# Performance work log

Measured on AMD Instinct MI355X. Metric: run time of the kernel, lower is better.

## Reference

```python
import jax, jax.numpy as jnp
import numpy as np
from jax import lax

D = 64
ROWS, COLS = np.triu_indices(D)  # 2080 upper-triangular (row, col) pairs, row-major like the python loop
BN_S = 1.0 / np.sqrt(1.0 + 1e-5)  # inference BN with running_mean=0, running_var=1


def _bn_relu(x, g, b):
    # inference-mode BatchNorm2d (fresh running stats) followed by ReLU; x is NCHW
    return jax.nn.relu(x * (g * BN_S)[None, :, None, None] + b[None, :, None, None])


def _conv(x, w, stride, pad):
    return lax.conv_general_dilated(x, w, (stride, stride), [(pad, pad), (pad, pad)],
                                    dimension_numbers=('NCHW', 'OIHW', 'NCHW'))


def _block(x, g1, b1, w1, g2, b2, w2, stride, ws=None):
    xa = _bn_relu(x, g1, b1)
    y = _conv(xa, w1, stride, 1)
    y = _conv(_bn_relu(y, g2, b2), w2, 1, 1)
    sc = xa if ws is None else _conv(xa, ws, stride, 0)
    return y + sc


def _forward(x, y, conv_w, s1_g1, s1_b1, s1_w1, s1_g2, s1_b2, s1_w2,
             s2_g1, s2_b1, s2_w1, s2_g2, s2_b2, s2_w2, s2_ws,
             s3_g1, s3_b1, s3_w1, s3_g2, s3_b2, s3_w2, s3_ws,
             bn_g, bn_b, ct_w, ct_b):
    h = _conv(x, conv_w, 1, 1)                                   # (B,16,36,60)
    h = _block(h, s1_g1, s1_b1, s1_w1, s1_g2, s1_b2, s1_w2, 1)    # (B,16,36,60)
    h = _block(h, s2_g1, s2_b1, s2_w1, s2_g2, s2_b2, s2_w2, 2, s2_ws)  # (B,32,18,30)
    h = _block(h, s3_g1, s3_b1, s3_w1, s3_g2, s3_b2, s3_w2, 2, s3_ws)  # (B,64,9,15)
    h = _bn_relu(h, bn_g, bn_b)                                   # (B,64,9,15)
    xp = jnp.transpose(h, (0, 2, 3, 1))                           # (B,9,15,64) channels-last
    # triangular bilinear pooling: z[..., k] = x[..., row_k] * x[..., col_k]
    z = xp[..., ROWS] * xp[..., COLS]                             # (B,9,15,2080)
    # 1x1 conv d2 -> 64 ("condtoc") + channel gating
    A = jnp.einsum('bhwk,ok->bhwo', z, ct_w) + ct_b               # (B,9,15,64)
    G = jnp.mean(A, axis=(1, 2), keepdims=True)                   # (B,1,1,64) adaptive avg pool
    Dg = A * G + A
    out = xp * Dg + xp                                            # (B,9,15,64)
    return out


def setup_inputs() -> dict:
    key = jax.random.key(0)
    ks = iter(jax.random.split(key, 40))

    def rn(shape, scale=0.1):
        return jax.random.normal(next(ks), shape, dtype=jnp.float32) * scale

    def gm(shape):
        return jax.random.uniform(next(ks), shape, dtype=jnp.float32, minval=0.5, maxval=1.5)

    return {
        'x': rn((64, 3, 36, 60), 1.0), 'y': rn((64, 2), 1.0),
        'conv_w': rn((16, 3, 3, 3)),
        's1_g1': gm((16,)), 's1_b1': rn((16,)), 's1_w1': rn((16, 16, 3, 3)),
        's1_g2': gm((16,)), 's1_b2': rn((16,)), 's1_w2': rn((16, 16, 3, 3)),
        's2_g1': gm((16,)), 's2_b1': rn((16,)), 's2_w1': rn((32, 16, 3, 3)),
        's2_g2': gm((32,)), 's2_b2': rn((32,)), 's2_w2': rn((32, 32, 3, 3)),
        's2_ws': rn((32, 16, 1, 1)),
        's3_g1': gm((32,)), 's3_b1': rn((32,)), 's3_w1': rn((64, 32, 3, 3)),
        's3_g2': gm((64,)), 's3_b2': rn((64,)), 's3_w2': rn((64, 64, 3, 3)),
        's3_ws': rn((64, 32, 1, 1)),
        'bn_g': gm((64,)), 'bn_b': rn((64,)),
        'ct_w': rn((64, 2080), 0.02), 'ct_b': rn((64,), 0.02),
    }


def reference(x, y, conv_w, s1_g1, s1_b1, s1_w1, s1_g2, s1_b2, s1_w2,
              s2_g1, s2_b1, s2_w1, s2_g2, s2_b2, s2_w2, s2_ws,
              s3_g1, s3_b1, s3_w1, s3_g2, s3_b2, s3_w2, s3_ws,
              bn_g, bn_b, ct_w, ct_b):
    return _forward(x, y, conv_w, s1_g1, s1_b1, s1_w1, s1_g2, s1_b2, s1_w2,
                    s2_g1, s2_b1, s2_w1, s2_g2, s2_b2, s2_w2, s2_ws,
                    s3_g1, s3_b1, s3_w1, s3_g2, s3_b2, s3_w2, s3_ws,
                    bn_g, bn_b, ct_w, ct_b)
```

## Files before the change

### kernel.cpp

```cpp
#include <hip/hip_runtime.h>

#define BN_S 0.9999950000374997f

constexpr int BATCH = 64;

typedef __attribute__((ext_vector_type(8))) short bf16x8;
typedef __attribute__((ext_vector_type(4))) float f32x4;

__device__ __forceinline__ float bnrelu(float x, float gs, float bb) {
    return fmaxf(fmaf(x, gs, bb), 0.f);
}

__device__ __forceinline__ unsigned short f2bf(float f) {
    unsigned u = __builtin_bit_cast(unsigned, f);
    return (unsigned short)((u + 0x7FFFu + ((u >> 16) & 1u)) >> 16);
}
__device__ __forceinline__ float bf2f(unsigned short h) {
    unsigned u = ((unsigned)h) << 16;
    return __builtin_bit_cast(float, u);
}

template<int CIN, int CICH, int COUT, int CO_PER, int HIN, int WIN,
         int HOUT, int WOUT, int STRIDE, int ROWS, int P, int PARTS,
         bool PRE_BN, int SC, int CSC, int SSTR, int SCPARTS>
__global__ __launch_bounds__(256) void convT_k(
    const float* __restrict__ in, size_t in_pstride,
    const float* __restrict__ w,
    const float* __restrict__ g, const float* __restrict__ bb,
    const float* __restrict__ xin, size_t xin_pstride,
    const float* __restrict__ g1v, const float* __restrict__ b1v,
    const float* __restrict__ wsc,
    float* __restrict__ out, size_t out_pstride)
{
    constexpr int IR = (STRIDE == 1) ? ROWS + 2 : 2 * ROWS + 1;
    constexpr int TW = (STRIDE == 1) ? WIN + 2 : WIN + 1;
    constexpr int AW = (P - 1) * STRIDE + 3;
    constexpr int NCOG = COUT / CO_PER;
    constexpr int PGW = WOUT / P;
    constexpr int NG = ROWS * PGW;
    constexpr int NITEMS = NG * NCOG;

    __shared__ float xs[CICH * IR * TW];
    __shared__ float wlds[CICH * 9 * COUT];
    __shared__ float g1l[SC ? CSC : 1], b1l[SC ? CSC : 1];
    __shared__ float wscl[(SC == 2) ? CSC * COUT : 1];

    const int band = blockIdx.x, b = blockIdx.y, zci = blockIdx.z;
    const int ci0 = zci * CICH;
    const int r0 = band * ROWS;
    const int r0in = r0 * STRIDE - 1;
    const int tid = threadIdx.x;

    for (int i = tid; i < CICH * 9 * COUT; i += 256) {
        int co = i % COUT; int rem = i / COUT; int tap = rem % 9; int ci = rem / 9;
        wlds[i] = w[((size_t)co * CIN + ci0 + ci) * 9 + tap];
    }
    if constexpr (SC != 0) {
        if (tid < CSC) { g1l[tid] = g1v[tid] * BN_S; b1l[tid] = b1v[tid]; }
        if constexpr (SC == 2) {
            for (int i = tid; i < CSC * COUT; i += 256) {
                int co = i % COUT; int ci = i / COUT;
                wscl[i] = wsc[(size_t)co * CSC + ci];
            }
        }
    }
    for (int i = tid; i < CICH * IR * TW; i += 256) {
        int cc = i % TW; int rem = i / TW; int rr = rem % IR; int ci = rem / IR;
        int gr = r0in + rr; int gc = cc - 1;
        float v = 0.f;
        if (gr >= 0 && gr < HIN && gc >= 0 && gc < WIN) {
            size_t off = ((size_t)(b * CIN + ci0 + ci) * HIN + gr) * WIN + gc;
            v = in[off];
            if constexpr (PARTS >= 2) v += in[off + in_pstride];
            if constexpr (PARTS >= 3) v += in[off + 2 * in_pstride];
            if constexpr (PARTS >= 4) v += in[off + 3 * in_pstride];
            if constexpr (PRE_BN) v = bnrelu(v, g[ci0 + ci] * BN_S, bb[ci0 + ci]);
        }
        xs[i] = v;
    }
    __syncthreads();

    for (int it = tid; it < NITEMS; it += 256) {
        const int cog = it / NG; const int gi = it % NG;
        const int lr = gi / PGW; const int wc = (gi % PGW) * P;
        float acc[P][CO_PER];
#pragma unroll
        for (int j = 0; j < P; ++j)
#pragma unroll
            for (int co = 0; co < CO_PER; ++co) acc[j][co] = 0.f;

        for (int ci = 0; ci < CICH; ++ci) {
            const float* xb = xs + ((ci * IR) + lr * STRIDE) * TW + wc * STRIDE;
#pragma unroll
            for (int dh = 0; dh < 3; ++dh) {
                float aw[AW];
#pragma unroll
                for (int a = 0; a < AW; ++a) aw[a] = xb[dh * TW + a];
#pragma unroll
                for (int dw = 0; dw < 3; ++dw) {
                    const float* wp = wlds + (ci * 9 + dh * 3 + dw) * COUT + cog * CO_PER;
#pragma unroll
                    for (int c4 = 0; c4 < CO_PER; c4 += 4) {
                        float4 wv = *(const float4*)(wp + c4);
#pragma unroll
                        for (int j = 0; j < P; ++j) {
                            float a_ = aw[j * STRIDE + dw];
                            acc[j][c4 + 0] = fmaf(a_, wv.x, acc[j][c4 + 0]);
                            acc[j][c4 + 1] = fmaf(a_, wv.y, acc[j][c4 + 1]);
                            acc[j][c4 + 2] = fmaf(a_, wv.z, acc[j][c4 + 2]);
                            acc[j][c4 + 3] = fmaf(a_, wv.w, acc[j][c4 + 3]);
                        }
                    }
                }
            }
        }

        if constexpr (SC == 1) {
            if (zci == 0) {
#pragma unroll
                for (int co = 0; co < CO_PER; ++co) {
                    int c = cog * CO_PER + co;
#pragma unroll
                    for (int j = 0; j < P; ++j) {
                        size_t off = ((size_t)(b * CSC + c) * HOUT + (r0 + lr)) * WOUT + wc + j;
                        float v = xin[off];
#pragma unroll
                        for (int s = 1; s < SCPARTS; ++s) v += xin[off + s * xin_pstride];
                        acc[j][co] += bnrelu(v, g1l[c], b1l[c]);
                    }
                }
            }
        }
        if constexpr (SC == 2) {
            if (zci == 0) {
                const int hix = (r0 + lr) * SSTR;
                for (int ci = 0; ci < CSC; ++ci) {
                    float vv[P];
#pragma unroll
                    for (int j = 0; j < P; ++j) {
                        size_t off = ((size_t)(b * CSC + ci) * (HOUT * SSTR) + hix) * (WOUT * SSTR)
                                     + (wc + j) * SSTR;
                        float v = xin[off];
#pragma unroll
                        for (int s = 1; s < SCPARTS; ++s) v += xin[off + s * xin_pstride];
                        vv[j] = bnrelu(v, g1l[ci], b1l[ci]);
                    }
                    const float* wp = wscl + ci * COUT + cog * CO_PER;
#pragma unroll
                    for (int c4 = 0; c4 < CO_PER; c4 += 4) {
                        float4 wv = *(const float4*)(wp + c4);
#pragma unroll
                        for (int j = 0; j < P; ++j) {
                            acc[j][c4 + 0] = fmaf(vv[j], wv.x, acc[j][c4 + 0]);
                            acc[j][c4 + 1] = fmaf(vv[j], wv.y, acc[j][c4 + 1]);
                            acc[j][c4 + 2] = fmaf(vv[j], wv.z, acc[j][c4 + 2]);
                            acc[j][c4 + 3] = fmaf(vv[j], wv.w, acc[j][c4 + 3]);
                        }
                    }
                }
            }
        }

        float* op = out + (size_t)zci * out_pstride
                    + ((size_t)(b * COUT + cog * CO_PER) * HOUT + (r0 + lr)) * WOUT + wc;
#pragma unroll
        for (int co = 0; co < CO_PER; ++co)
#pragma unroll
            for (int j = 0; j < P; ++j)
                op[(size_t)co * HOUT * WOUT + j] = acc[j][co];
    }
}

__global__ void f0_k(const float* __restrict__ ctw, short* __restrict__ wf)
{
    int id = blockIdx.x * 256 + threadIdx.x;
    int j = id & 7; int lane = (id >> 3) & 63; int tile = (id >> 9) & 3; int s = id >> 11;
    int c, ch;
    if (s < 32) { c = s; ch = 0; }
    else { c = 32 + ((s - 32) >> 1); ch = (s - 32) & 1; }
    int k = ch * 32 + ((lane >> 4) << 3) + j;
    int o = tile * 16 + (lane & 15);
    float val = 0.f;
    if (k <= c) val = ctw[o * 2080 + (k * (129 - k)) / 2 + (c - k)];
    wf[id] = (short)f2bf(val);
}

__global__ __launch_bounds__(256) void red_k(
    const float* __restrict__ pb, const float* __restrict__ h2,
    const float* __restrict__ g1, const float* __restrict__ b1,
    const float* __restrict__ wsc, const float* __restrict__ bng,
    const float* __restrict__ bnb, float* __restrict__ xp)
{
    __shared__ float hsc[32][136];
    __shared__ float wscl[32][16];
    __shared__ float g1l[32], b1l[32];
    const int b = blockIdx.x, cq = blockIdx.y;
    const int c0 = cq * 16;
    const int t = threadIdx.x;

    if (t < 32) { g1l[t] = g1[t] * BN_S; b1l[t] = b1[t]; }
    for (int i = t; i < 512; i += 256) {
        int ci = i & 31, cc = i >> 5;
        wscl[ci][cc] = wsc[(size_t)(c0 + cc) * 32 + ci];
    }
    __syncthreads();
    for (int i = t; i < 32 * 135; i += 256) {
        int ci = i / 135, p = i % 135;
        int hp = p / 15, wp = p % 15;
        size_t off = ((size_t)(b * 32 + ci) * 18 + hp * 2) * 30 + wp * 2;
        float v = h2[off] + h2[off + 1105920] + h2[off + 2 * 1105920] + h2[off + 3 * 1105920];
        hsc[ci][p] = bnrelu(v, g1l[ci], b1l[ci]);
    }
    __syncthreads();

    for (int e = t; e < 16 * 135; e += 256) {
        int cc = e / 135, p = e % 135;
        int c = c0 + cc;
        size_t idx = ((size_t)(b * 64 + c)) * 135 + p;
        float y = 0.f;
#pragma unroll
        for (int q = 0; q < 8; ++q) y += pb[idx + (size_t)q * 552960];
#pragma unroll 8
        for (int ci = 0; ci < 32; ++ci) y = fmaf(hsc[ci][p], wscl[ci][cc], y);
        xp[((size_t)b * 135 + p) * 64 + c] = bnrelu(y, bng[c] * BN_S, bnb[c]);
    }
}

template<int NCH>
__device__ __forceinline__ void f2m_body(
    const unsigned short* xs, int q, const short* __restrict__ wf,
    const float* __restrict__ ctb, float* __restrict__ Abase, int p0, int t)
{
    float* A = Abase + (size_t)q * 552960;
    const int w = t >> 6, lane = t & 63;
    const int prow = w * 32;
    const int lrow = lane & 15, lk = lane >> 4;

    bf16x8 Af[2][NCH];
#pragma unroll
    for (int rt = 0; rt < 2; ++rt)
#pragma unroll
        for (int ch = 0; ch < NCH; ++ch) {
            int pix = prow + rt * 16 + lrow;
            int g = ch * 4 + lk;
            Af[rt][ch] = *(const bf16x8*)&xs[pix * 64 + ((g ^ (pix & 7)) * 8)];
        }

    f32x4 acc[2][4];
#pragma unroll
    for (int rt = 0; rt < 2; ++rt)
#pragma unroll
        for (int tt = 0; tt < 4; ++tt) acc[rt][tt] = f32x4{0.f, 0.f, 0.f, 0.f};

    const int c0 = q * 16;
    bf16x8 BA[NCH][4], BB[NCH][4];

    auto loadB = [&](int c, bf16x8 (&B)[NCH][4]) {
        int slotb = (NCH == 1) ? c : (2 * c - 32);
#pragma unroll
        for (int ch = 0; ch < NCH; ++ch) {
            const short* wb = wf + (size_t)(slotb + ch) * 2048 + lane * 8;
#pragma unroll
            for (int tt = 0; tt < 4; ++tt)
                B[ch][tt] = *(const bf16x8*)(wb + tt * 512);
        }
    };
    auto compute = [&](int c, bf16x8 (&B)[NCH][4]) {
        f32x4 S[2][4];
#pragma unroll
        for (int rt = 0; rt < 2; ++rt)
#pragma unroll
            for (int tt = 0; tt < 4; ++tt) S[rt][tt] = f32x4{0.f, 0.f, 0.f, 0.f};
#pragma unroll
        for (int ch = 0; ch < NCH; ++ch)
#pragma unroll
            for (int tt = 0; tt < 4; ++tt) {
                S[0][tt] = __builtin_amdgcn_mfma_f32_16x16x32_bf16(Af[0][ch], B[ch][tt], S[0][tt], 0, 0, 0);
                S[1][tt] = __builtin_amdgcn_mfma_f32_16x16x32_bf16(Af[1][ch], B[ch][tt], S[1][tt], 0, 0, 0);
            }
#pragma unroll
        for (int rt = 0; rt < 2; ++rt)
#pragma unroll
            for (int j = 0; j < 4; ++j) {
                int pix = prow + rt * 16 + lk * 4 + j;
                float sv = bf2f(xs[pix * 64 + (((c >> 3) ^ (pix & 7)) * 8) + (c & 7)]);
#pragma unroll
                for (int tt = 0; tt < 4; ++tt)
                    acc[rt][tt][j] += sv * S[rt][tt][j];
            }
    };

    loadB(c0, BA);
#pragma unroll 1
    for (int ci = 0; ci < 16; ci += 2) {
        loadB(c0 + ci + 1, BB);
        compute(c0 + ci, BA);
        if (ci < 14) loadB(c0 + ci + 2, BA);
        compute(c0 + ci + 1, BB);
    }

#pragma unroll
    for (int rt = 0; rt < 2; ++rt)
#pragma unroll
        for (int j = 0; j < 4; ++j) {
            int gpix = p0 + prow + rt * 16 + lk * 4 + j;
            if (gpix < 8640) {
#pragma unroll
                for (int tt = 0; tt < 4; ++tt) {
                    int o = tt * 16 + lrow;
                    float vv = acc[rt][tt][j];
                    if (q == 0) vv += ctb[o];
                    A[(size_t)gpix * 64 + o] = vv;
                }
            }
        }
}

__global__ __launch_bounds__(256) void f2m_k(
    const float* __restrict__ xp, const short* __restrict__ wf,
    const float* __restrict__ ctb, float* __restrict__ Abase)
{
    __shared__ unsigned short xs[128 * 64];
    const int t = threadIdx.x;
    const int p0 = blockIdx.x * 128;
    const int q = blockIdx.y;

    {
        int pr = t >> 1, h = t & 1;
        int gp = p0 + pr;
        float v[32];
        if (gp < 8640) {
            const float4* src = (const float4*)(xp + (size_t)gp * 64 + h * 32);
#pragma unroll
            for (int i = 0; i < 8; ++i) {
                float4 x4 = src[i];
                v[i*4+0] = x4.x; v[i*4+1] = x4.y; v[i*4+2] = x4.z; v[i*4+3] = x4.w;
            }
        } else {
#pragma unroll
            for (int i = 0; i < 32; ++i) v[i] = 0.f;
        }
#pragma unroll
        for (int g = 0; g < 4; ++g) {
            unsigned w0 = f2bf(v[g*8+0]) | ((unsigned)f2bf(v[g*8+1]) << 16);
            unsigned w1 = f2bf(v[g*8+2]) | ((unsigned)f2bf(v[g*8+3]) << 16);
            unsigned w2 = f2bf(v[g*8+4]) | ((unsigned)f2bf(v[g*8+5]) << 16);
            unsigned w3 = f2bf(v[g*8+6]) | ((unsigned)f2bf(v[g*8+7]) << 16);
            int grp = h * 4 + g;
            int sg = grp ^ (pr & 7);
            *(uint4*)&xs[pr * 64 + sg * 8] = make_uint4(w0, w1, w2, w3);
        }
    }
    __syncthreads();

    if (q < 2) f2m_body<1>(xs, q, wf, ctb, Abase, p0, t);
    else       f2m_body<2>(xs, q, wf, ctb, Abase, p0, t);
}

__global__ void f3a_k(const float* __restrict__ A, float* __restrict__ G)
{
    int b = blockIdx.x; int t = threadIdx.x;
    int o = t & 63; int grp = t >> 6;
    float s = 0.f;
    for (int p = grp; p < 135; p += 4) {
        size_t off = ((size_t)b * 135 + p) * 64 + o;
        s += A[off] + A[off + 552960] + A[off + 2 * 552960] + A[off + 3 * 552960];
    }
    __shared__ float red[4][64];
    red[grp][o] = s;
    __syncthreads();
    if (t < 64) G[b * 64 + t] = (red[0][t] + red[1][t] + red[2][t] + red[3][t]) * (1.0f / 135.0f);
}

__global__ void f3b_k(const float* __restrict__ xp, const float* __restrict__ A,
                      const float* __restrict__ G, float* __restrict__ out)
{
    int idx = blockIdx.x * 256 + threadIdx.x;
    if (idx >= BATCH * 135 * 64) return;
    int o = idx & 63; int b = idx / (135 * 64);
    float a = A[idx] + A[idx + 552960] + A[idx + 2 * 552960] + A[idx + 3 * 552960];
    float g = G[b * 64 + o];
    float x = xp[idx];
    out[idx] = fmaf(x, a * (g + 1.f), x);
}

extern "C" void kernel_launch(void* const* d_in, const int* in_sizes, int n_in,
                              void* d_out, int out_size, void* d_ws, size_t ws_size,
                              hipStream_t stream)
{
    const float* x      = (const float*)d_in[0];
    const float* conv_w = (const float*)d_in[2];
    const float* s1_g1  = (const float*)d_in[3];
    const float* s1_b1  = (const float*)d_in[4];
    const float* s1_w1  = (const float*)d_in[5];
    const float* s1_g2  = (const float*)d_in[6];
    const float* s1_b2  = (const float*)d_in[7];
    const float* s1_w2  = (const float*)d_in[8];
    const float* s2_g1  = (const float*)d_in[9];
    const float* s2_b1  = (const float*)d_in[10];
    const float* s2_w1  = (const float*)d_in[11];
    const float* s2_g2  = (const float*)d_in[12];
    const float* s2_b2  = (const float*)d_in[13];
    const float* s2_w2  = (const float*)d_in[14];
    const float* s2_ws  = (const float*)d_in[15];
    const float* s3_g1  = (const float*)d_in[16];
    const float* s3_b1  = (const float*)d_in[17];
    const float* s3_w1  = (const float*)d_in[18];
    const float* s3_g2  = (const float*)d_in[19];
    const float* s3_b2  = (const float*)d_in[20];
    const float* s3_w2  = (const float*)d_in[21];
    const float* s3_ws  = (const float*)d_in[22];
    const float* bn_g   = (const float*)d_in[23];
    const float* bn_b   = (const float*)d_in[24];
    const float* ct_w   = (const float*)d_in[25];
    const float* ct_b   = (const float*)d_in[26];
    float* out = (float*)d_out;

    float* ws = (float*)d_ws;
    float* h0      = ws + 0;
    float* p_b1c1  = ws + 2211840;
    float* h1      = ws + 11059200;
    float* p_b2c1  = ws + 0;
    float* p_b2c2  = ws + 4423680;
    float* p_b3c1  = ws + 0;
    float* p_b3c2  = ws + 8847360;
    float* xp      = ws + 0;
    float* A       = ws + 552960;
    float* G       = ws + 15482880;
    short* wfrag   = (short*)(ws + 15487232);

    dim3 blk(256);

    f0_k<<<768, blk, 0, stream>>>(ct_w, wfrag);

    convT_k<3, 3, 16, 8, 36, 60, 36, 60, 1, 6, 3, 1, false, 0, 1, 1, 1>
        <<<dim3(6, 64, 1), blk, 0, stream>>>(
        x, 0, conv_w, nullptr, nullptr, nullptr, 0, nullptr, nullptr, nullptr, h0, 0);
    convT_k<16, 4, 16, 8, 36, 60, 36, 60, 1, 9, 5, 1, true, 0, 1, 1, 1>
        <<<dim3(4, 64, 4), blk, 0, stream>>>(
        h0, 0, s1_w1, s1_g1, s1_b1, nullptr, 0, nullptr, nullptr, nullptr, p_b1c1, 2211840);
    convT_k<16, 8, 16, 8, 36, 60, 36, 60, 1, 9, 5, 4, true, 1, 16, 1, 1>
        <<<dim3(4, 64, 2), blk, 0, stream>>>(
        p_b1c1, 2211840, s1_w2, s1_g2, s1_b2, h0, 0, s1_g1, s1_b1, nullptr, h1, 2211840);
    convT_k<16, 4, 32, 8, 36, 60, 18, 30, 2, 6, 5, 2, true, 0, 1, 1, 1>
        <<<dim3(3, 64, 4), blk, 0, stream>>>(
        h1, 2211840, s2_w1, s2_g1, s2_b1, nullptr, 0, nullptr, nullptr, nullptr, p_b2c1, 1105920);
    convT_k<32, 8, 32, 8, 18, 30, 18, 30, 1, 6, 5, 4, true, 2, 16, 2, 2>
        <<<dim3(3, 64, 4), blk, 0, stream>>>(
        p_b2c1, 1105920, s2_w2, s2_g2, s2_b2, h1, 2211840, s2_g1, s2_b1, s2_ws, p_b2c2, 1105920);
    convT_k<32, 8, 64, 4, 18, 30, 9, 15, 2, 3, 3, 4, true, 0, 1, 1, 1>
        <<<dim3(3, 64, 4), blk, 0, stream>>>(
        p_b2c2, 1105920, s3_w1, s3_g1, s3_b1, nullptr, 0, nullptr, nullptr, nullptr, p_b3c1, 552960);
    convT_k<64, 8, 64, 4, 9, 15, 9, 15, 1, 3, 3, 4, true, 0, 1, 1, 1>
        <<<dim3(3, 64, 8), blk, 0, stream>>>(
        p_b3c1, 552960, s3_w2, s3_g2, s3_b2, nullptr, 0, nullptr, nullptr, nullptr, p_b3c2, 552960);
    red_k<<<dim3(64, 4), blk, 0, stream>>>(p_b3c2, p_b2c2,
                                           s3_g1, s3_b1, s3_ws, bn_g, bn_b, xp);
    f2m_k<<<dim3(68, 4), blk, 0, stream>>>(xp, wfrag, ct_b, A);

    f3a_k<<<64, blk, 0, stream>>>(A, G);
    f3b_k<<<2160, blk, 0, stream>>>(xp, A, G, out);
}
```

Baseline: 202.7 us.

## Merge prep kernels, retile early convs, fuse gating kernels, separate workspace buffers

```diff
diff --git a/kernel.cpp b/kernel.cpp
--- a/kernel.cpp
+++ b/kernel.cpp
@@ -18,6 +18,156 @@
 __device__ __forceinline__ float bf2f(unsigned short h) {
     unsigned u = ((unsigned)h) << 16;
     return __builtin_bit_cast(float, u);
+}
+
+template<int CIN, int CICH, int COUT, int CO_PER, int HIN, int WIN,
+         int HOUT, int WOUT, int STRIDE, int ROWS, int P, int PARTS,
+         bool PRE_BN, int SC, int CSC, int SSTR, int SCPARTS>
+__device__ void convT_tile(float* smem, int band, int b, int zci,
+    const float* __restrict__ in, size_t in_pstride,
+    const float* __restrict__ w,
+    const float* __restrict__ g, const float* __restrict__ bb,
+    const float* __restrict__ xin, size_t xin_pstride,
+    const float* __restrict__ g1v, const float* __restrict__ b1v,
+    const float* __restrict__ wsc,
+    float* __restrict__ out, size_t out_pstride)
+{
+    constexpr int IR = (STRIDE == 1) ? ROWS + 2 : 2 * ROWS + 1;
+    constexpr int TW = (STRIDE == 1) ? WIN + 2 : WIN + 1;
+    constexpr int AW = (P - 1) * STRIDE + 3;
+    constexpr int PGW = WOUT / P;
+    constexpr int NG = ROWS * PGW;
+    constexpr int NITEMS = NG * (COUT / CO_PER);
+
+    float* xs   = smem;
+    float* wlds = xs + CICH * IR * TW;
+    float* wscl = wlds + CICH * 9 * COUT;
+    float* g1l  = wscl + ((SC == 2) ? CSC * COUT : 0);
+    float* b1l  = g1l + (SC ? CSC : 0);
+
+    const int ci0 = zci * CICH;
+    const int r0 = band * ROWS;
+    const int r0in = r0 * STRIDE - 1;
+    const int tid = threadIdx.x;
+
+    for (int i = tid; i < CICH * 9 * COUT; i += 256) {
+        int co = i % COUT; int rem = i / COUT; int tap = rem % 9; int ci = rem / 9;
+        wlds[i] = w[((size_t)co * CIN + ci0 + ci) * 9 + tap];
+    }
+    if constexpr (SC != 0) {
+        if (tid < CSC) { g1l[tid] = g1v[tid] * BN_S; b1l[tid] = b1v[tid]; }
+        if constexpr (SC == 2) {
+            for (int i = tid; i < CSC * COUT; i += 256) {
+                int co = i % COUT; int ci = i / COUT;
+                wscl[i] = wsc[(size_t)co * CSC + ci];
+            }
+        }
+    }
+    for (int i = tid; i < CICH * IR * TW; i += 256) {
+        int cc = i % TW; int rem = i / TW; int rr = rem % IR; int ci = rem / IR;
+        int gr = r0in + rr; int gc = cc - 1;
+        float v = 0.f;
+        if (gr >= 0 && gr < HIN && gc >= 0 && gc < WIN) {
+            size_t off = ((size_t)(b * CIN + ci0 + ci) * HIN + gr) * WIN + gc;
+            v = in[off];
+#pragma unroll
+            for (int s = 1; s < PARTS; ++s) v += in[off + (size_t)s * in_pstride];
+            if constexpr (PRE_BN) v = bnrelu(v, g[ci0 + ci] * BN_S, bb[ci0 + ci]);
+        }
+        xs[i] = v;
+    }
+    __syncthreads();
+
+    if (tid < NITEMS) {
+        const int it = tid;
+        const int cog = it / NG; const int gi = it % NG;
+        const int lr = gi / PGW; const int wc = (gi % PGW) * P;
+        float acc[P][CO_PER];
+#pragma unroll
+        for (int j = 0; j < P; ++j)
+#pragma unroll
+            for (int co = 0; co < CO_PER; ++co) acc[j][co] = 0.f;
+
+        for (int ci = 0; ci < CICH; ++ci) {
+            const float* xb = xs + ((ci * IR) + lr * STRIDE) * TW + wc * STRIDE;
+#pragma unroll
+            for (int dh = 0; dh < 3; ++dh) {
+                float aw[AW];
+#pragma unroll
+                for (int a = 0; a < AW; ++a) aw[a] = xb[dh * TW + a];
+#pragma unroll
+                for (int dw = 0; dw < 3; ++dw) {
+                    const float* wp = wlds + (ci * 9 + dh * 3 + dw) * COUT + cog * CO_PER;
+#pragma unroll
+                    for (int c4 = 0; c4 < CO_PER; c4 += 4) {
+                        float4 wv = *(const float4*)(wp + c4);
+#pragma unroll
+                        for (int j = 0; j < P; ++j) {
+                            float a_ = aw[j * STRIDE + dw];
+                            acc[j][c4 + 0] = fmaf(a_, wv.x, acc[j][c4 + 0]);
+                            acc[j][c4 + 1] = fmaf(a_, wv.y, acc[j][c4 + 1]);
+                            acc[j][c4 + 2] = fmaf(a_, wv.z, acc[j][c4 + 2]);
+                            acc[j][c4 + 3] = fmaf(a_, wv.w, acc[j][c4 + 3]);
+                        }
+                    }
+                }
+            }
+        }
+
+        if constexpr (SC == 1) {
+            if (zci == 0) {
+#pragma unroll
+                for (int co = 0; co < CO_PER; ++co) {
+                    int c = cog * CO_PER + co;
+#pragma unroll
+                    for (int j = 0; j < P; ++j) {
+                        size_t off = ((size_t)(b * CSC + c) * HOUT + (r0 + lr)) * WOUT + wc + j;
+                        float v = xin[off];
+#pragma unroll
+                        for (int s = 1; s < SCPARTS; ++s) v += xin[off + s * xin_pstride];
+                        acc[j][co] += bnrelu(v, g1l[c], b1l[c]);
+                    }
+                }
+            }
+        }
+        if constexpr (SC == 2) {
+            if (zci == 0) {
+                const int hix = (r0 + lr) * SSTR;
+                for (int ci = 0; ci < CSC; ++ci) {
+                    float vv[P];
+#pragma unroll
+                    for (int j = 0; j < P; ++j) {
+                        size_t off = ((size_t)(b * CSC + ci) * (HOUT * SSTR) + hix) * (WOUT * SSTR)
+                                     + (wc + j) * SSTR;
+                        float v = xin[off];
+#pragma unroll
+                        for (int s = 1; s < SCPARTS; ++s) v += xin[off + s * xin_pstride];
+                        vv[j] = bnrelu(v, g1l[ci], b1l[ci]);
+                    }
+                    const float* wp = wscl + ci * COUT + cog * CO_PER;
+#pragma unroll
+                    for (int c4 = 0; c4 < CO_PER; c4 += 4) {
+                        float4 wv = *(const float4*)(wp + c4);
+#pragma unroll
+                        for (int j = 0; j < P; ++j) {
+                            acc[j][c4 + 0] = fmaf(vv[j], wv.x, acc[j][c4 + 0]);
+                            acc[j][c4 + 1] = fmaf(vv[j], wv.y, acc[j][c4 + 1]);
+                            acc[j][c4 + 2] = fmaf(vv[j], wv.z, acc[j][c4 + 2]);
+                            acc[j][c4 + 3] = fmaf(vv[j], wv.w, acc[j][c4 + 3]);
+                        }
+                    }
+                }
+            }
+        }
+
+        float* op = out + (size_t)zci * out_pstride
+                    + ((size_t)(b * COUT + cog * CO_PER) * HOUT + (r0 + lr)) * WOUT + wc;
+#pragma unroll
+        for (int co = 0; co < CO_PER; ++co)
+#pragma unroll
+            for (int j = 0; j < P; ++j)
+                op[(size_t)co * HOUT * WOUT + j] = acc[j][co];
+    }
 }
 
 template<int CIN, int CICH, int COUT, int CO_PER, int HIN, int WIN,
@@ -34,155 +184,39 @@
 {
     constexpr int IR = (STRIDE == 1) ? ROWS + 2 : 2 * ROWS + 1;
     constexpr int TW = (STRIDE == 1) ? WIN + 2 : WIN + 1;
-    constexpr int AW = (P - 1) * STRIDE + 3;
-    constexpr int NCOG = COUT / CO_PER;
-    constexpr int PGW = WOUT / P;
-    constexpr int NG = ROWS * PGW;
-    constexpr int NITEMS = NG * NCOG;
-
-    __shared__ float xs[CICH * IR * TW];
-    __shared__ float wlds[CICH * 9 * COUT];
-    __shared__ float g1l[SC ? CSC : 1], b1l[SC ? CSC : 1];
-    __shared__ float wscl[(SC == 2) ? CSC * COUT : 1];
-
-    const int band = blockIdx.x, b = blockIdx.y, zci = blockIdx.z;
-    const int ci0 = zci * CICH;
-    const int r0 = band * ROWS;
-    const int r0in = r0 * STRIDE - 1;
-    const int tid = threadIdx.x;
-
-    for (int i = tid; i < CICH * 9 * COUT; i += 256) {
-        int co = i % COUT; int rem = i / COUT; int tap = rem % 9; int ci = rem / 9;
-        wlds[i] = w[((size_t)co * CIN + ci0 + ci) * 9 + tap];
-    }
-    if constexpr (SC != 0) {
-        if (tid < CSC) { g1l[tid] = g1v[tid] * BN_S; b1l[tid] = b1v[tid]; }
-        if constexpr (SC == 2) {
-            for (int i = tid; i < CSC * COUT; i += 256) {
-                int co = i % COUT; int ci = i / COUT;
-                wscl[i] = wsc[(size_t)co * CSC + ci];
-            }
-        }
-    }
-    for (int i = tid; i < CICH * IR * TW; i += 256) {
-        int cc = i % TW; int rem = i / TW; int rr = rem % IR; int ci = rem / IR;
-        int gr = r0in + rr; int gc = cc - 1;
-        float v = 0.f;
-        if (gr >= 0 && gr < HIN && gc >= 0 && gc < WIN) {
-            size_t off = ((size_t)(b * CIN + ci0 + ci) * HIN + gr) * WIN + gc;
-            v = in[off];
-            if constexpr (PARTS >= 2) v += in[off + in_pstride];
-            if constexpr (PARTS >= 3) v += in[off + 2 * in_pstride];
-            if constexpr (PARTS >= 4) v += in[off + 3 * in_pstride];
-            if constexpr (PRE_BN) v = bnrelu(v, g[ci0 + ci] * BN_S, bb[ci0 + ci]);
-        }
-        xs[i] = v;
-    }
-    __syncthreads();
-
-    for (int it = tid; it < NITEMS; it += 256) {
-        const int cog = it / NG; const int gi = it % NG;
-        const int lr = gi / PGW; const int wc = (gi % PGW) * P;
-        float acc[P][CO_PER];
-#pragma unroll
-        for (int j = 0; j < P; ++j)
-#pragma unroll
-            for (int co = 0; co < CO_PER; ++co) acc[j][co] = 0.f;
-
-        for (int ci = 0; ci < CICH; ++ci) {
-            const float* xb = xs + ((ci * IR) + lr * STRIDE) * TW + wc * STRIDE;
-#pragma unroll
-            for (int dh = 0; dh < 3; ++dh) {
-                float aw[AW];
-#pragma unroll
-                for (int a = 0; a < AW; ++a) aw[a] = xb[dh * TW + a];
-#pragma unroll
-                for (int dw = 0; dw < 3; ++dw) {
-                    const float* wp = wlds + (ci * 9 + dh * 3 + dw) * COUT + cog * CO_PER;
-#pragma unroll
-                    for (int c4 = 0; c4 < CO_PER; c4 += 4) {
-                        float4 wv = *(const float4*)(wp + c4);
-#pragma unroll
-                        for (int j = 0; j < P; ++j) {
-                            float a_ = aw[j * STRIDE + dw];
-                            acc[j][c4 + 0] = fmaf(a_, wv.x, acc[j][c4 + 0]);
-                            acc[j][c4 + 1] = fmaf(a_, wv.y, acc[j][c4 + 1]);
-                            acc[j][c4 + 2] = fmaf(a_, wv.z, acc[j][c4 + 2]);
-                            acc[j][c4 + 3] = fmaf(a_, wv.w, acc[j][c4 + 3]);
-                        }
-                    }
-                }
-            }
-        }
-
-        if constexpr (SC == 1) {
-            if (zci == 0) {
-#pragma unroll
-                for (int co = 0; co < CO_PER; ++co) {
-                    int c = cog * CO_PER + co;
-#pragma unroll
-                    for (int j = 0; j < P; ++j) {
-                        size_t off = ((size_t)(b * CSC + c) * HOUT + (r0 + lr)) * WOUT + wc + j;
-                        float v = xin[off];
-#pragma unroll
-                        for (int s = 1; s < SCPARTS; ++s) v += xin[off + s * xin_pstride];
-                        acc[j][co] += bnrelu(v, g1l[c], b1l[c]);
-                    }
-                }
-            }
-        }
-        if constexpr (SC == 2) {
-            if (zci == 0) {
-                const int hix = (r0 + lr) * SSTR;
-                for (int ci = 0; ci < CSC; ++ci) {
-                    float vv[P];
-#pragma unroll
-                    for (int j = 0; j < P; ++j) {
-                        size_t off = ((size_t)(b * CSC + ci) * (HOUT * SSTR) + hix) * (WOUT * SSTR)
-                                     + (wc + j) * SSTR;
-                        float v = xin[off];
-#pragma unroll
-                        for (int s = 1; s < SCPARTS; ++s) v += xin[off + s * xin_pstride];
-                        vv[j] = bnrelu(v, g1l[ci], b1l[ci]);
-                    }
-                    const float* wp = wscl + ci * COUT + cog * CO_PER;
-#pragma unroll
-                    for (int c4 = 0; c4 < CO_PER; c4 += 4) {
-                        float4 wv = *(const float4*)(wp + c4);
-#pragma unroll
-                        for (int j = 0; j < P; ++j) {
-                            acc[j][c4 + 0] = fmaf(vv[j], wv.x, acc[j][c4 + 0]);
-                            acc[j][c4 + 1] = fmaf(vv[j], wv.y, acc[j][c4 + 1]);
-                            acc[j][c4 + 2] = fmaf(vv[j], wv.z, acc[j][c4 + 2]);
-                            acc[j][c4 + 3] = fmaf(vv[j], wv.w, acc[j][c4 + 3]);
-                        }
-                    }
-                }
-            }
-        }
-
-        float* op = out + (size_t)zci * out_pstride
-                    + ((size_t)(b * COUT + cog * CO_PER) * HOUT + (r0 + lr)) * WOUT + wc;
-#pragma unroll
-        for (int co = 0; co < CO_PER; ++co)
-#pragma unroll
-            for (int j = 0; j < P; ++j)
-                op[(size_t)co * HOUT * WOUT + j] = acc[j][co];
-    }
-}
-
-__global__ void f0_k(const float* __restrict__ ctw, short* __restrict__ wf)
-{
-    int id = blockIdx.x * 256 + threadIdx.x;
-    int j = id & 7; int lane = (id >> 3) & 63; int tile = (id >> 9) & 3; int s = id >> 11;
-    int c, ch;
-    if (s < 32) { c = s; ch = 0; }
-    else { c = 32 + ((s - 32) >> 1); ch = (s - 32) & 1; }
-    int k = ch * 32 + ((lane >> 4) << 3) + j;
-    int o = tile * 16 + (lane & 15);
-    float val = 0.f;
-    if (k <= c) val = ctw[o * 2080 + (k * (129 - k)) / 2 + (c - k)];
-    wf[id] = (short)f2bf(val);
+    constexpr int SM = CICH * IR * TW + CICH * 9 * COUT
+                     + ((SC == 2) ? CSC * COUT : 0) + (SC ? 2 * CSC : 0);
+    __shared__ __align__(16) float smem[SM];
+    convT_tile<CIN, CICH, COUT, CO_PER, HIN, WIN, HOUT, WOUT, STRIDE, ROWS, P,
+               PARTS, PRE_BN, SC, CSC, SSTR, SCPARTS>(
+        smem, blockIdx.x, blockIdx.y, blockIdx.z,
+        in, in_pstride, w, g, bb, xin, xin_pstride, g1v, b1v, wsc, out, out_pstride);
+}
+
+__global__ __launch_bounds__(256) void prep_k(
+    const float* __restrict__ ctw, short* __restrict__ wf,
+    const float* __restrict__ x, const float* __restrict__ conv_w,
+    float* __restrict__ h0)
+{
+    __shared__ __align__(16) float smem[3 * 8 * 62 + 3 * 9 * 16];
+    int tl = blockIdx.x;
+    if (tl < 768) {
+        int id = tl * 256 + threadIdx.x;
+        int j = id & 7; int lane = (id >> 3) & 63; int t4 = (id >> 9) & 3; int s = id >> 11;
+        int c, ch;
+        if (s < 32) { c = s; ch = 0; }
+        else { c = 32 + ((s - 32) >> 1); ch = (s - 32) & 1; }
+        int k = ch * 32 + ((lane >> 4) << 3) + j;
+        int o = t4 * 16 + (lane & 15);
+        float val = 0.f;
+        if (k <= c) val = ctw[o * 2080 + (k * (129 - k)) / 2 + (c - k)];
+        wf[id] = (short)f2bf(val);
+    } else {
+        int tt = tl - 768;
+        convT_tile<3, 3, 16, 8, 36, 60, 36, 60, 1, 6, 3, 1, false, 0, 1, 1, 1>(
+            smem, tt % 6, tt / 6, 0, x, 0, conv_w, nullptr, nullptr,
+            nullptr, 0, nullptr, nullptr, nullptr, h0, 0);
+    }
 }
 
 __global__ __launch_bounds__(256) void red_k(
@@ -227,7 +261,7 @@
 }
 
 template<int NCH>
-__device__ __forceinline__ void f2m_body(
+__device__ void f2m_body(
     const unsigned short* xs, int q, const short* __restrict__ wf,
     const float* __restrict__ ctb, float* __restrict__ Abase, int p0, int t)
 {
@@ -357,31 +391,35 @@
     else       f2m_body<2>(xs, q, wf, ctb, Abase, p0, t);
 }
 
-__global__ void f3a_k(const float* __restrict__ A, float* __restrict__ G)
-{
-    int b = blockIdx.x; int t = threadIdx.x;
-    int o = t & 63; int grp = t >> 6;
+__global__ __launch_bounds__(256) void f3_k(
+    const float* __restrict__ xp, const float* __restrict__ A,
+    float* __restrict__ out)
+{
+    __shared__ float red[256];
+    __shared__ float gG[64];
+    const int b = blockIdx.x;
+    const int t = threadIdx.x;
+    const int o = t & 63, grp = t >> 6;
+
     float s = 0.f;
     for (int p = grp; p < 135; p += 4) {
         size_t off = ((size_t)b * 135 + p) * 64 + o;
         s += A[off] + A[off + 552960] + A[off + 2 * 552960] + A[off + 3 * 552960];
     }
-    __shared__ float red[4][64];
-    red[grp][o] = s;
+    red[grp * 64 + o] = s;
     __syncthreads();
-    if (t < 64) G[b * 64 + t] = (red[0][t] + red[1][t] + red[2][t] + red[3][t]) * (1.0f / 135.0f);
-}
-
-__global__ void f3b_k(const float* __restrict__ xp, const float* __restrict__ A,
-                      const float* __restrict__ G, float* __restrict__ out)
-{
-    int idx = blockIdx.x * 256 + threadIdx.x;
-    if (idx >= BATCH * 135 * 64) return;
-    int o = idx & 63; int b = idx / (135 * 64);
-    float a = A[idx] + A[idx + 552960] + A[idx + 2 * 552960] + A[idx + 3 * 552960];
-    float g = G[b * 64 + o];
-    float x = xp[idx];
-    out[idx] = fmaf(x, a * (g + 1.f), x);
+    if (t < 64)
+        gG[t] = (red[t] + red[64 + t] + red[128 + t] + red[192 + t]) * (1.0f / 135.0f);
+    __syncthreads();
+
+    const size_t base = (size_t)b * 8640;
+    for (int e = t; e < 8640; e += 256) {
+        size_t idx = base + e;
+        int oo = e & 63;
+        float a = A[idx] + A[idx + 552960] + A[idx + 2 * 552960] + A[idx + 3 * 552960];
+        float x = xp[idx];
+        out[idx] = fmaf(x, a * (gG[oo] + 1.f), x);
+    }
 }
 
 extern "C" void kernel_launch(void* const* d_in, const int* in_sizes, int n_in,
@@ -419,45 +457,45 @@
     float* ws = (float*)d_ws;
     float* h0      = ws + 0;
     float* p_b1c1  = ws + 2211840;
-    float* h1      = ws + 11059200;
-    float* p_b2c1  = ws + 0;
-    float* p_b2c2  = ws + 4423680;
-    float* p_b3c1  = ws + 0;
-    float* p_b3c2  = ws + 8847360;
-    float* xp      = ws + 0;
-    float* A       = ws + 552960;
-    float* G       = ws + 15482880;
-    short* wfrag   = (short*)(ws + 15487232);
+    float* h1      = ws + 6635520;
+    float* p_b2c1  = ws + 8847360;
+    float* p_b2c2  = ws + 11059200;
+    float* p_b3c1  = ws + 15482880;
+    float* p_b3c2  = ws + 17694720;
+    float* xp      = ws + 22118400;
+    float* A       = ws + 22671360;
+    short* wfrag   = (short*)(ws + 24883200);
 
     dim3 blk(256);
 
-    f0_k<<<768, blk, 0, stream>>>(ct_w, wfrag);
-
-    convT_k<3, 3, 16, 8, 36, 60, 36, 60, 1, 6, 3, 1, false, 0, 1, 1, 1>
-        <<<dim3(6, 64, 1), blk, 0, stream>>>(
-        x, 0, conv_w, nullptr, nullptr, nullptr, 0, nullptr, nullptr, nullptr, h0, 0);
-    convT_k<16, 4, 16, 8, 36, 60, 36, 60, 1, 9, 5, 1, true, 0, 1, 1, 1>
-        <<<dim3(4, 64, 4), blk, 0, stream>>>(
-        h0, 0, s1_w1, s1_g1, s1_b1, nullptr, 0, nullptr, nullptr, nullptr, p_b1c1, 2211840);
-    convT_k<16, 8, 16, 8, 36, 60, 36, 60, 1, 9, 5, 4, true, 1, 16, 1, 1>
-        <<<dim3(4, 64, 2), blk, 0, stream>>>(
-        p_b1c1, 2211840, s1_w2, s1_g2, s1_b2, h0, 0, s1_g1, s1_b1, nullptr, h1, 2211840);
-    convT_k<16, 4, 32, 8, 36, 60, 18, 30, 2, 6, 5, 2, true, 0, 1, 1, 1>
-        <<<dim3(3, 64, 4), blk, 0, stream>>>(
-        h1, 2211840, s2_w1, s2_g1, s2_b1, nullptr, 0, nullptr, nullptr, nullptr, p_b2c1, 1105920);
-    convT_k<32, 8, 32, 8, 18, 30, 18, 30, 1, 6, 5, 4, true, 2, 16, 2, 2>
-        <<<dim3(3, 64, 4), blk, 0, stream>>>(
-        p_b2c1, 1105920, s2_w2, s2_g2, s2_b2, h1, 2211840, s2_g1, s2_b1, s2_ws, p_b2c2, 1105920);
+    prep_k<<<1152, blk, 0, stream>>>(ct_w, wfrag, x, conv_w, h0);
+
+    convT_k<16, 8, 16, 4, 36, 60, 36, 60, 1, 4, 5, 1, true, 0, 1, 1, 1>
+        <<<dim3(9, 64, 2), blk, 0, stream>>>(
+        h0, 0, s1_w1, s1_g1, s1_b1, nullptr, 0, nullptr, nullptr, nullptr,
+        p_b1c1, 2211840);
+    convT_k<16, 16, 16, 4, 36, 60, 36, 60, 1, 4, 5, 2, true, 1, 16, 1, 1>
+        <<<dim3(9, 64, 1), blk, 0, stream>>>(
+        p_b1c1, 2211840, s1_w2, s1_g2, s1_b2, h0, 0, s1_g1, s1_b1, nullptr,
+        h1, 0);
+    convT_k<16, 8, 32, 4, 36, 60, 18, 30, 2, 3, 3, 1, true, 0, 1, 1, 1>
+        <<<dim3(6, 64, 2), blk, 0, stream>>>(
+        h1, 0, s2_w1, s2_g1, s2_b1, nullptr, 0, nullptr, nullptr, nullptr,
+        p_b2c1, 1105920);
+    convT_k<32, 8, 32, 4, 18, 30, 18, 30, 1, 3, 3, 2, true, 2, 16, 2, 1>
+        <<<dim3(6, 64, 4), blk, 0, stream>>>(
+        p_b2c1, 1105920, s2_w2, s2_g2, s2_b2, h1, 0, s2_g1, s2_b1, s2_ws,
+        p_b2c2, 1105920);
     convT_k<32, 8, 64, 4, 18, 30, 9, 15, 2, 3, 3, 4, true, 0, 1, 1, 1>
         <<<dim3(3, 64, 4), blk, 0, stream>>>(
-        p_b2c2, 1105920, s3_w1, s3_g1, s3_b1, nullptr, 0, nullptr, nullptr, nullptr, p_b3c1, 552960);
+        p_b2c2, 1105920, s3_w1, s3_g1, s3_b1, nullptr, 0, nullptr, nullptr, nullptr,
+        p_b3c1, 552960);
     convT_k<64, 8, 64, 4, 9, 15, 9, 15, 1, 3, 3, 4, true, 0, 1, 1, 1>
         <<<dim3(3, 64, 8), blk, 0, stream>>>(
-        p_b3c1, 552960, s3_w2, s3_g2, s3_b2, nullptr, 0, nullptr, nullptr, nullptr, p_b3c2, 552960);
+        p_b3c1, 552960, s3_w2, s3_g2, s3_b2, nullptr, 0, nullptr, nullptr, nullptr,
+        p_b3c2, 552960);
     red_k<<<dim3(64, 4), blk, 0, stream>>>(p_b3c2, p_b2c2,
                                            s3_g1, s3_b1, s3_ws, bn_g, bn_b, xp);
     f2m_k<<<dim3(68, 4), blk, 0, stream>>>(xp, wfrag, ct_b, A);
-
-    f3a_k<<<64, blk, 0, stream>>>(A, G);
-    f3b_k<<<2160, blk, 0, stream>>>(xp, A, G, out);
-}
+    f3_k<<<64, blk, 0, stream>>>(xp, A, out);
+}
```

Result: no change. 200.1 us (-1.3%).
